# Kernel tuning notes

Measured on AMD Instinct MI355X. Metric: run time of the kernel, lower is better.

The kernel has to match this reference:

```python
import jax, jax.numpy as jnp
import numpy as np

B, N, F_IN, F_OUT = 8, 2048, 64, 64
ALPHA = 0.2  # LeakyReLU negative slope
LN_EPS = 1e-5
NEG_BIG = -9e15


def setup_inputs() -> dict:
    key = jax.random.key(0)
    ks = jax.random.split(key, 8)
    inp = {}
    inp["input"] = jax.random.normal(ks[0], (B, N, F_IN), dtype=jnp.float32)
    inp["adj"] = jax.random.randint(ks[1], (N, N), 0, 2, dtype=jnp.int32)
    # parameters (kaiming/xavier approximated with scaled normals)
    inp["W"] = jax.random.normal(ks[2], (F_IN, F_OUT), dtype=jnp.float32) * np.sqrt(2.0 / F_OUT)
    inp["a"] = jax.random.normal(ks[3], (2 * F_OUT, 1), dtype=jnp.float32) * np.sqrt(2.0 / (2 * F_OUT + 1))
    inp["node_weights"] = jax.random.normal(ks[4], (N,), dtype=jnp.float32)
    inp["node_bias"] = jnp.zeros((N,), dtype=jnp.float32)
    inp["ln_gamma"] = jnp.ones((F_OUT,), dtype=jnp.float32)
    inp["ln_beta"] = jnp.zeros((F_OUT,), dtype=jnp.float32)
    return inp


def reference(input, adj, W, a, node_weights, node_bias, ln_gamma, ln_beta):
    # eval mode: dropout is identity
    # node-wise affine + residual
    x = input * node_weights[None, :, None] + node_bias[None, :, None] + input
    # linear projection + LayerNorm over features
    h = jnp.matmul(x, W)  # [B, N, F_OUT]
    mu = jnp.mean(h, axis=-1, keepdims=True)
    var = jnp.mean(jnp.square(h - mu), axis=-1, keepdims=True)
    h = (h - mu) * jax.lax.rsqrt(var + LN_EPS) * ln_gamma + ln_beta
    # additive GAT scores WITHOUT materializing [B,N,N,2F]:
    # e_ij = LeakyReLU(h_i . a1 + h_j . a2), identical math to cat([h_i,h_j]) @ a
    a1 = a[:F_OUT, 0]
    a2 = a[F_OUT:, 0]
    s1 = jnp.einsum("bnf,f->bn", h, a1)  # [B, N]
    s2 = jnp.einsum("bnf,f->bn", h, a2)  # [B, N]
    e = jax.nn.leaky_relu(s1[:, :, None] + s2[:, None, :], negative_slope=ALPHA)
    # masked softmax over neighbors (last axis)
    mask = (adj > 0)[None, :, :]  # [1, N, N] broadcast over batch
    att = jax.nn.softmax(jnp.where(mask, e, NEG_BIG), axis=-1)
    # weighted aggregation + residual, then ELU (concat=True)
    h_prime = jnp.matmul(att, h) + h
    return jax.nn.elu(h_prime)
```

## Files before the change

### kernel.cpp

```cpp
#include <hip/hip_runtime.h>
#include <math.h>

#define Bb 8
#define Nn 2048
#define ALPHA 0.2f
#define LN_EPS 1e-5f
#define LOG2E 1.4426950408889634f

typedef __attribute__((ext_vector_type(8))) short short8;
typedef __attribute__((ext_vector_type(4))) float f32x4;
typedef __attribute__((ext_vector_type(4))) int int4v;

__device__ inline unsigned short f2bf(float f) {
    unsigned u = __builtin_bit_cast(unsigned, f);
    u += 0x7fffu + ((u >> 16) & 1u);
    return (unsigned short)(u >> 16);
}

__device__ __forceinline__ void gll16(const void* g, void* l) {
    __builtin_amdgcn_global_load_lds(
        (const __attribute__((address_space(1))) unsigned int*)g,
        (__attribute__((address_space(3))) unsigned int*)l, 16, 0, 0);
}

__global__ __launch_bounds__(256) void pack_mask(const int* __restrict__ adj,
                                                 unsigned int* __restrict__ bitsT) {
    int g = blockIdx.x * blockDim.x + threadIdx.x;
    int lane = threadIdx.x & 63;
    int pred = adj[g] > 0;
    unsigned long long b = __ballot(pred);
    if ((lane & 31) == 0) {
        unsigned w32 = (unsigned)(b >> (lane & 32));
        int i = g >> 11, w = (g >> 5) & 63;
        bitsT[((size_t)(i >> 4) * 64 + w) * 16 + (i & 15)] = w32;
    }
}

__global__ __launch_bounds__(64) void node_transform_mfma(
    const float* __restrict__ in, const float* __restrict__ W,
    const float* __restrict__ a, const float* __restrict__ nw,
    const float* __restrict__ nb, const float* __restrict__ gam,
    const float* __restrict__ bet,
    float* __restrict__ h, float* __restrict__ s1L, float* __restrict__ s2L,
    unsigned short* __restrict__ hT2)
{
    int lane = threadIdx.x;
    int am = lane & 15, ag = lane >> 4;
    int node0 = blockIdx.x * 16;
    int b = node0 >> 11;
    int n0 = node0 & (Nn - 1);

    short8 wf[4][2];
#pragma unroll
    for (int cb = 0; cb < 4; ++cb)
#pragma unroll
        for (int kh = 0; kh < 2; ++kh)
#pragma unroll
            for (int e = 0; e < 8; ++e)
                wf[cb][kh][e] = (short)f2bf(W[(kh * 32 + 8 * ag + e) * 64 + cb * 16 + am]);

    int nrow = n0 + am;
    float nwv = nw[nrow] + 1.0f, nbv = nb[nrow];
    const float* xrow = in + (size_t)(node0 + am) * 64 + 8 * ag;
    short8 xa0, xa1;
#pragma unroll
    for (int e = 0; e < 8; ++e) {
        xa0[e] = (short)f2bf(xrow[e] * nwv + nbv);
        xa1[e] = (short)f2bf(xrow[32 + e] * nwv + nbv);
    }

    f32x4 acc0 = {0,0,0,0}, acc1 = {0,0,0,0}, acc2 = {0,0,0,0}, acc3 = {0,0,0,0};
    acc0 = __builtin_amdgcn_mfma_f32_16x16x32_bf16(xa0, wf[0][0], acc0, 0, 0, 0);
    acc1 = __builtin_amdgcn_mfma_f32_16x16x32_bf16(xa0, wf[1][0], acc1, 0, 0, 0);
    acc2 = __builtin_amdgcn_mfma_f32_16x16x32_bf16(xa0, wf[2][0], acc2, 0, 0, 0);
    acc3 = __builtin_amdgcn_mfma_f32_16x16x32_bf16(xa0, wf[3][0], acc3, 0, 0, 0);
    acc0 = __builtin_amdgcn_mfma_f32_16x16x32_bf16(xa1, wf[0][1], acc0, 0, 0, 0);
    acc1 = __builtin_amdgcn_mfma_f32_16x16x32_bf16(xa1, wf[1][1], acc1, 0, 0, 0);
    acc2 = __builtin_amdgcn_mfma_f32_16x16x32_bf16(xa1, wf[2][1], acc2, 0, 0, 0);
    acc3 = __builtin_amdgcn_mfma_f32_16x16x32_bf16(xa1, wf[3][1], acc3, 0, 0, 0);

    float mu[4], rsq[4];
#pragma unroll
    for (int q = 0; q < 4; ++q) {
        float s = (acc0[q] + acc1[q]) + (acc2[q] + acc3[q]);
        s += __shfl_xor(s, 1, 64); s += __shfl_xor(s, 2, 64);
        s += __shfl_xor(s, 4, 64); s += __shfl_xor(s, 8, 64);
        mu[q] = s * (1.f / 64.f);
    }
#pragma unroll
    for (int q = 0; q < 4; ++q) {
        float d0 = acc0[q] - mu[q], d1 = acc1[q] - mu[q];
        float d2 = acc2[q] - mu[q], d3 = acc3[q] - mu[q];
        float ss = (d0 * d0 + d1 * d1) + (d2 * d2 + d3 * d3);
        ss += __shfl_xor(ss, 1, 64); ss += __shfl_xor(ss, 2, 64);
        ss += __shfl_xor(ss, 4, 64); ss += __shfl_xor(ss, 8, 64);
        rsq[q] = rsqrtf(ss * (1.f / 64.f) + LN_EPS);
    }
    float gl0 = gam[am], gl1 = gam[16 + am], gl2 = gam[32 + am], gl3 = gam[48 + am];
    float bl0 = bet[am], bl1 = bet[16 + am], bl2 = bet[32 + am], bl3 = bet[48 + am];
    f32x4 hn0, hn1, hn2, hn3;
#pragma unroll
    for (int q = 0; q < 4; ++q) {
        hn0[q] = (acc0[q] - mu[q]) * rsq[q] * gl0 + bl0;
        hn1[q] = (acc1[q] - mu[q]) * rsq[q] * gl1 + bl1;
        hn2[q] = (acc2[q] - mu[q]) * rsq[q] * gl2 + bl2;
        hn3[q] = (acc3[q] - mu[q]) * rsq[q] * gl3 + bl3;
    }

    float a10 = a[am], a11 = a[16 + am], a12 = a[32 + am], a13 = a[48 + am];
    float a20 = a[64 + am], a21 = a[80 + am], a22 = a[96 + am], a23 = a[112 + am];
    float s1p[4], s2p[4];
#pragma unroll
    for (int q = 0; q < 4; ++q) {
        float s1v = (hn0[q] * a10 + hn1[q] * a11) + (hn2[q] * a12 + hn3[q] * a13);
        float s2v = (hn0[q] * a20 + hn1[q] * a21) + (hn2[q] * a22 + hn3[q] * a23);
        s1v += __shfl_xor(s1v, 1, 64); s1v += __shfl_xor(s1v, 2, 64);
        s1v += __shfl_xor(s1v, 4, 64); s1v += __shfl_xor(s1v, 8, 64);
        s2v += __shfl_xor(s2v, 1, 64); s2v += __shfl_xor(s2v, 2, 64);
        s2v += __shfl_xor(s2v, 4, 64); s2v += __shfl_xor(s2v, 8, 64);
        s1p[q] = s1v; s2p[q] = s2v;
    }
    if (am == 0) {
#pragma unroll
        for (int q = 0; q < 4; ++q) {
            s1L[node0 + ag * 4 + q] = s1p[q] * LOG2E;
            s2L[node0 + ag * 4 + q] = s2p[q] * LOG2E;
        }
    }

#pragma unroll
    for (int q = 0; q < 4; ++q) {
        float* hp = h + (size_t)(node0 + ag * 4 + q) * 64 + am;
        hp[0] = hn0[q]; hp[16] = hn1[q]; hp[32] = hn2[q]; hp[48] = hn3[q];
    }

    int jw = n0 >> 5;
    int AG2 = ((n0 & 31) >> 3) + (ag >> 1);
    int e0 = (ag & 1) * 4;
    size_t fbase = ((size_t)((b * 64 + jw) * 4)) * 512 + (AG2 * 16 + am) * 8 + e0;
#pragma unroll
    for (int cb = 0; cb < 4; ++cb) {
        f32x4 hc = cb == 0 ? hn0 : cb == 1 ? hn1 : cb == 2 ? hn2 : hn3;
        unsigned short v[4] = {f2bf(hc[0]), f2bf(hc[1]), f2bf(hc[2]), f2bf(hc[3])};
        *(uint2*)&hT2[fbase + (size_t)cb * 512] = *(uint2*)v;
    }
}

__global__ __launch_bounds__(256, 4) void attention8(
    const unsigned short* __restrict__ hT2,
    const float* __restrict__ s1L, const float* __restrict__ s2L,
    const unsigned int* __restrict__ bitsT,
    float* __restrict__ pacc, float* __restrict__ pz)
{
    __shared__ __align__(16) unsigned short frag[2][4][4][512];
    __shared__ __align__(16) unsigned int mask_lds[2][32][16];
    __shared__ __align__(16) float s2l[1024];

    int t = threadIdx.x, wv = t >> 6, lane = t & 63;
    int am = lane & 15, ag = lane >> 4;
    int rr = wv & 1, js = wv >> 1;
    int bx = blockIdx.x, jh = blockIdx.y, b = blockIdx.z;

    float s1r = s1L[b * Nn + bx * 32 + rr * 16 + am];
    const unsigned short* slab = hT2 + (size_t)b * 131072;

    {
        const unsigned int* msrc = bitsT
            + ((size_t)(bx * 2 + (wv >> 1)) * 64 + jh * 32) * 16 + (wv & 1) * 256;
        gll16(msrc + lane * 4, &((unsigned int*)mask_lds)[wv * 256]);
        gll16(s2L + b * Nn + jh * 1024 + wv * 256 + lane * 4, &s2l[wv * 256]);
    }
    {
        const unsigned short* wsrc = slab + ((size_t)(jh * 32 + wv) * 4) * 512;
#pragma unroll
        for (int fb = 0; fb < 4; ++fb)
            gll16(wsrc + fb * 512 + lane * 8, &frag[0][wv][fb][0]);
    }
    asm volatile("s_waitcnt vmcnt(0)" ::: "memory");
    __builtin_amdgcn_s_barrier();

    f32x4 acc0 = {0,0,0,0}, acc1 = {0,0,0,0}, acc2 = {0,0,0,0}, acc3 = {0,0,0,0};
    f32x4 accz = {0,0,0,0};
    const short8 vone = {(short)0x3F80, (short)0x3F80, (short)0x3F80, (short)0x3F80,
                         (short)0x3F80, (short)0x3F80, (short)0x3F80, (short)0x3F80};

#pragma unroll
    for (int st = 0; st < 8; ++st) {
        if (st < 7) {
            const unsigned short* wsrc =
                slab + ((size_t)(jh * 32 + (st + 1) * 4 + wv) * 4) * 512;
#pragma unroll
            for (int fb = 0; fb < 4; ++fb)
                gll16(wsrc + fb * 512 + lane * 8, &frag[(st + 1) & 1][wv][fb][0]);
        }
#pragma unroll
        for (int wi = 0; wi < 2; ++wi) {
            int wls = js * 2 + wi;
            int wl = st * 4 + wls;
            unsigned wd = mask_lds[rr][wl][am];
            float4 sa = *(const float4*)&s2l[wl * 32 + 8 * ag];
            float4 sb = *(const float4*)&s2l[wl * 32 + 8 * ag + 4];
            float se[8] = {sa.x, sa.y, sa.z, sa.w, sb.x, sb.y, sb.z, sb.w};
            float p[8];
#pragma unroll
            for (int e = 0; e < 8; ++e) {
                float x = s1r + se[e];
                float lr = fmaxf(x, ALPHA * x);
                float ev = __builtin_amdgcn_exp2f(lr);
                p[e] = ((wd >> (8 * ag + e)) & 1u) ? ev : 0.f;
            }
            int4v aw;
            aw.x = __builtin_amdgcn_perm(__builtin_bit_cast(unsigned, p[1]),
                                         __builtin_bit_cast(unsigned, p[0]), 0x07060302u);
            aw.y = __builtin_amdgcn_perm(__builtin_bit_cast(unsigned, p[3]),
                                         __builtin_bit_cast(unsigned, p[2]), 0x07060302u);
            aw.z = __builtin_amdgcn_perm(__builtin_bit_cast(unsigned, p[5]),
                                         __builtin_bit_cast(unsigned, p[4]), 0x07060302u);
            aw.w = __builtin_amdgcn_perm(__builtin_bit_cast(unsigned, p[7]),
                                         __builtin_bit_cast(unsigned, p[6]), 0x07060302u);
            short8 af = __builtin_bit_cast(short8, aw);
            short8 f0 = *(const short8*)&frag[st & 1][wls][0][lane * 8];
            short8 f1 = *(const short8*)&frag[st & 1][wls][1][lane * 8];
            short8 f2 = *(const short8*)&frag[st & 1][wls][2][lane * 8];
            short8 f3 = *(const short8*)&frag[st & 1][wls][3][lane * 8];
            acc0 = __builtin_amdgcn_mfma_f32_16x16x32_bf16(af, f0, acc0, 0, 0, 0);
            acc1 = __builtin_amdgcn_mfma_f32_16x16x32_bf16(af, f1, acc1, 0, 0, 0);
            acc2 = __builtin_amdgcn_mfma_f32_16x16x32_bf16(af, f2, acc2, 0, 0, 0);
            acc3 = __builtin_amdgcn_mfma_f32_16x16x32_bf16(af, f3, acc3, 0, 0, 0);
            accz = __builtin_amdgcn_mfma_f32_16x16x32_bf16(af, vone, accz, 0, 0, 0);
        }
        asm volatile("s_waitcnt vmcnt(0)" ::: "memory");
        __builtin_amdgcn_s_barrier();
    }

    float* ep  = (float*)&frag[0][0][0][0];
    float* zep = (float*)&frag[1][0][0][0];
#pragma unroll
    for (int q = 0; q < 4; ++q) {
        int rloc = rr * 16 + 4 * ag + q;
        ep[(js * 32 + rloc) * 64 +  0 + am] = acc0[q];
        ep[(js * 32 + rloc) * 64 + 16 + am] = acc1[q];
        ep[(js * 32 + rloc) * 64 + 32 + am] = acc2[q];
        ep[(js * 32 + rloc) * 64 + 48 + am] = acc3[q];
        if (am == 0) zep[js * 32 + rloc] = accz[q];
    }
    __syncthreads();

    int rl = t >> 3, fo = (t & 7) * 8;
    float zsum = zep[rl] + zep[32 + rl];
    const float* e0p = &ep[rl * 64 + fo];
    const float* e1p = &ep[(32 + rl) * 64 + fo];
    size_t prow = (size_t)(b * 2 + jh) * 2048 + bx * 32 + rl;
    float4 v0, v1;
    v0.x = e0p[0] + e1p[0]; v0.y = e0p[1] + e1p[1];
    v0.z = e0p[2] + e1p[2]; v0.w = e0p[3] + e1p[3];
    v1.x = e0p[4] + e1p[4]; v1.y = e0p[5] + e1p[5];
    v1.z = e0p[6] + e1p[6]; v1.w = e0p[7] + e1p[7];
    *(float4*)&pacc[prow * 64 + fo]     = v0;
    *(float4*)&pacc[prow * 64 + fo + 4] = v1;
    if ((t & 7) == 0) pz[prow] = zsum;
}

__global__ __launch_bounds__(256) void combine(
    const float* __restrict__ pacc, const float* __restrict__ pz,
    const float* __restrict__ h, float* __restrict__ out)
{
    int u = blockIdx.x * 256 + threadIdx.x;
    int fq = u & 15, grow = u >> 4;
    int b = grow >> 11, i = grow & 2047;
    size_t p0 = ((size_t)(b * 2) * 2048 + i) * 64 + fq * 4;
    float4 a0 = *(const float4*)&pacc[p0];
    float4 a1 = *(const float4*)&pacc[p0 + (size_t)2048 * 64];
    float z = pz[(size_t)(b * 2) * 2048 + i] + pz[(size_t)(b * 2 + 1) * 2048 + i];
    float zinv = 1.f / z;
    size_t ob = (size_t)grow * 64 + fq * 4;
    float4 hv = *(const float4*)&h[ob];
    float4 o;
    o.x = (a0.x + a1.x) * zinv + hv.x; o.x = o.x > 0.f ? o.x : expm1f(o.x);
    o.y = (a0.y + a1.y) * zinv + hv.y; o.y = o.y > 0.f ? o.y : expm1f(o.y);
    o.z = (a0.z + a1.z) * zinv + hv.z; o.z = o.z > 0.f ? o.z : expm1f(o.z);
    o.w = (a0.w + a1.w) * zinv + hv.w; o.w = o.w > 0.f ? o.w : expm1f(o.w);
    *(float4*)&out[ob] = o;
}

extern "C" void kernel_launch(void* const* d_in, const int* in_sizes, int n_in,
                              void* d_out, int out_size, void* d_ws, size_t ws_size,
                              hipStream_t stream) {
    const float* in  = (const float*)d_in[0];
    const int*   adj = (const int*)d_in[1];
    const float* W   = (const float*)d_in[2];
    const float* a   = (const float*)d_in[3];
    const float* nw  = (const float*)d_in[4];
    const float* nb  = (const float*)d_in[5];
    const float* gam = (const float*)d_in[6];
    const float* bet = (const float*)d_in[7];
    float* out = (float*)d_out;

    char* ws = (char*)d_ws;
    float* h   = (float*)ws;
    float* s1L = (float*)(ws + (size_t)Bb * Nn * 64 * 4);
    float* s2L = s1L + (size_t)Bb * Nn;
    unsigned int* bitsT = (unsigned int*)(s2L + (size_t)Bb * Nn);
    unsigned short* hT2 = (unsigned short*)(bitsT + (size_t)Nn * Nn / 32);
    float* pacc = (float*)(hT2 + (size_t)Bb * 64 * Nn);
    float* pz   = pacc + (size_t)16 * 2048 * 64;

    hipLaunchKernelGGL(pack_mask, dim3(Nn * Nn / 256), dim3(256), 0, stream, adj, bitsT);
    hipLaunchKernelGGL(node_transform_mfma, dim3(Bb * Nn / 16), dim3(64), 0, stream,
                       in, W, a, nw, nb, gam, bet, h, s1L, s2L, hT2);
    hipLaunchKernelGGL(attention8, dim3(Nn / 32, 2, Bb), dim3(256), 0, stream,
                       hT2, s1L, s2L, bitsT, pacc, pz);
    hipLaunchKernelGGL(combine, dim3((Bb * Nn * 16) / 256), dim3(256), 0, stream,
                       pacc, pz, h, out);
}
```

Baseline: 36.07 us.

## Fuse mask packing with node transform and fold combine into attention

Mask packing and the node transform now run as one launch, with extra blocks handling adjacency rows through vectorized int4 loads and an LDS byte gather. The attention kernel drops the split over the neighbor dimension, so each block loops over all 2048 neighbors in 16 stages. It also applies the normalization, residual and ELU directly, which removes the partial-sum buffers and the separate combine kernel. In exchange there are half as many attention blocks (512 instead of 1024) with larger LDS use and the occupancy hint removed, which may reduce latency hiding.

```diff
diff --git a/kernel.cpp b/kernel.cpp
--- a/kernel.cpp
+++ b/kernel.cpp
@@ -23,30 +23,40 @@
         (__attribute__((address_space(3))) unsigned int*)l, 16, 0, 0);
 }
 
-__global__ __launch_bounds__(256) void pack_mask(const int* __restrict__ adj,
-                                                 unsigned int* __restrict__ bitsT) {
-    int g = blockIdx.x * blockDim.x + threadIdx.x;
-    int lane = threadIdx.x & 63;
-    int pred = adj[g] > 0;
-    unsigned long long b = __ballot(pred);
-    if ((lane & 31) == 0) {
-        unsigned w32 = (unsigned)(b >> (lane & 32));
-        int i = g >> 11, w = (g >> 5) & 63;
-        bitsT[((size_t)(i >> 4) * 64 + w) * 16 + (i & 15)] = w32;
-    }
-}
-
-__global__ __launch_bounds__(64) void node_transform_mfma(
+__global__ __launch_bounds__(256) void prep(
+    const int* __restrict__ adj,
     const float* __restrict__ in, const float* __restrict__ W,
     const float* __restrict__ a, const float* __restrict__ nw,
     const float* __restrict__ nb, const float* __restrict__ gam,
     const float* __restrict__ bet,
+    unsigned int* __restrict__ bitsT,
     float* __restrict__ h, float* __restrict__ s1L, float* __restrict__ s2L,
     unsigned short* __restrict__ hT2)
 {
-    int lane = threadIdx.x;
+    __shared__ unsigned char rowb[256];
+    int bid = blockIdx.x, t = threadIdx.x;
+
+    if (bid < Nn) {
+        int i = bid;
+        const int4* arow = (const int4*)(adj + (size_t)i * Nn);
+        int4 v0 = arow[t * 2], v1 = arow[t * 2 + 1];
+        unsigned by = (unsigned)(v0.x > 0)       | ((unsigned)(v0.y > 0) << 1)
+                    | ((unsigned)(v0.z > 0) << 2) | ((unsigned)(v0.w > 0) << 3)
+                    | ((unsigned)(v1.x > 0) << 4) | ((unsigned)(v1.y > 0) << 5)
+                    | ((unsigned)(v1.z > 0) << 6) | ((unsigned)(v1.w > 0) << 7);
+        rowb[t] = (unsigned char)by;
+        __syncthreads();
+        if (t < 64) {
+            unsigned w32;
+            __builtin_memcpy(&w32, &rowb[t * 4], 4);
+            bitsT[((size_t)(i >> 4) * 64 + t) * 16 + (i & 15)] = w32;
+        }
+        return;
+    }
+
+    int lane = t & 63, wv = t >> 6;
     int am = lane & 15, ag = lane >> 4;
-    int node0 = blockIdx.x * 16;
+    int node0 = (bid - Nn) * 64 + wv * 16;
     int b = node0 >> 11;
     int n0 = node0 & (Nn - 1);
 
@@ -146,36 +156,34 @@
     }
 }
 
-__global__ __launch_bounds__(256, 4) void attention8(
-    const unsigned short* __restrict__ hT2,
+__global__ __launch_bounds__(256) void attention9(
+    const float* __restrict__ h, const unsigned short* __restrict__ hT2,
     const float* __restrict__ s1L, const float* __restrict__ s2L,
-    const unsigned int* __restrict__ bitsT,
-    float* __restrict__ pacc, float* __restrict__ pz)
+    const unsigned int* __restrict__ bitsT, float* __restrict__ out)
 {
     __shared__ __align__(16) unsigned short frag[2][4][4][512];
-    __shared__ __align__(16) unsigned int mask_lds[2][32][16];
-    __shared__ __align__(16) float s2l[1024];
+    __shared__ __align__(16) unsigned int mask_lds[2][64][16];
+    __shared__ __align__(16) float s2l[2048];
 
     int t = threadIdx.x, wv = t >> 6, lane = t & 63;
     int am = lane & 15, ag = lane >> 4;
     int rr = wv & 1, js = wv >> 1;
-    int bx = blockIdx.x, jh = blockIdx.y, b = blockIdx.z;
+    int bx = blockIdx.x, b = blockIdx.y;
 
     float s1r = s1L[b * Nn + bx * 32 + rr * 16 + am];
+    const unsigned int* msrc = bitsT + (size_t)(bx * 2) * 1024;
+    const float* ssrc = s2L + b * Nn;
     const unsigned short* slab = hT2 + (size_t)b * 131072;
 
-    {
-        const unsigned int* msrc = bitsT
-            + ((size_t)(bx * 2 + (wv >> 1)) * 64 + jh * 32) * 16 + (wv & 1) * 256;
-        gll16(msrc + lane * 4, &((unsigned int*)mask_lds)[wv * 256]);
-        gll16(s2L + b * Nn + jh * 1024 + wv * 256 + lane * 4, &s2l[wv * 256]);
-    }
-    {
-        const unsigned short* wsrc = slab + ((size_t)(jh * 32 + wv) * 4) * 512;
-#pragma unroll
-        for (int fb = 0; fb < 4; ++fb)
-            gll16(wsrc + fb * 512 + lane * 8, &frag[0][wv][fb][0]);
-    }
+#pragma unroll
+    for (int k = 0; k < 2; ++k) {
+        int sl = wv * 2 + k;
+        gll16(msrc + sl * 256 + lane * 4, &((unsigned int*)mask_lds)[sl * 256]);
+        gll16(ssrc + sl * 256 + lane * 4, &s2l[sl * 256]);
+    }
+#pragma unroll
+    for (int fb = 0; fb < 4; ++fb)
+        gll16(slab + (size_t)(wv * 4 + fb) * 512 + lane * 8, &frag[0][wv][fb][0]);
     asm volatile("s_waitcnt vmcnt(0)" ::: "memory");
     __builtin_amdgcn_s_barrier();
 
@@ -185,13 +193,13 @@
                          (short)0x3F80, (short)0x3F80, (short)0x3F80, (short)0x3F80};
 
 #pragma unroll
-    for (int st = 0; st < 8; ++st) {
-        if (st < 7) {
-            const unsigned short* wsrc =
-                slab + ((size_t)(jh * 32 + (st + 1) * 4 + wv) * 4) * 512;
+    for (int st = 0; st < 16; ++st) {
+        if (st < 15) {
+            int gw = (st + 1) * 4 + wv;
 #pragma unroll
             for (int fb = 0; fb < 4; ++fb)
-                gll16(wsrc + fb * 512 + lane * 8, &frag[(st + 1) & 1][wv][fb][0]);
+                gll16(slab + (size_t)(gw * 4 + fb) * 512 + lane * 8,
+                      &frag[(st + 1) & 1][wv][fb][0]);
         }
 #pragma unroll
         for (int wi = 0; wi < 2; ++wi) {
@@ -247,40 +255,23 @@
     __syncthreads();
 
     int rl = t >> 3, fo = (t & 7) * 8;
-    float zsum = zep[rl] + zep[32 + rl];
+    float zinv = 1.f / (zep[rl] + zep[32 + rl]);
+    size_t base = ((size_t)(b * Nn + bx * 32 + rl)) * 64 + fo;
     const float* e0p = &ep[rl * 64 + fo];
     const float* e1p = &ep[(32 + rl) * 64 + fo];
-    size_t prow = (size_t)(b * 2 + jh) * 2048 + bx * 32 + rl;
-    float4 v0, v1;
-    v0.x = e0p[0] + e1p[0]; v0.y = e0p[1] + e1p[1];
-    v0.z = e0p[2] + e1p[2]; v0.w = e0p[3] + e1p[3];
-    v1.x = e0p[4] + e1p[4]; v1.y = e0p[5] + e1p[5];
-    v1.z = e0p[6] + e1p[6]; v1.w = e0p[7] + e1p[7];
-    *(float4*)&pacc[prow * 64 + fo]     = v0;
-    *(float4*)&pacc[prow * 64 + fo + 4] = v1;
-    if ((t & 7) == 0) pz[prow] = zsum;
-}
-
-__global__ __launch_bounds__(256) void combine(
-    const float* __restrict__ pacc, const float* __restrict__ pz,
-    const float* __restrict__ h, float* __restrict__ out)
-{
-    int u = blockIdx.x * 256 + threadIdx.x;
-    int fq = u & 15, grow = u >> 4;
-    int b = grow >> 11, i = grow & 2047;
-    size_t p0 = ((size_t)(b * 2) * 2048 + i) * 64 + fq * 4;
-    float4 a0 = *(const float4*)&pacc[p0];
-    float4 a1 = *(const float4*)&pacc[p0 + (size_t)2048 * 64];
-    float z = pz[(size_t)(b * 2) * 2048 + i] + pz[(size_t)(b * 2 + 1) * 2048 + i];
-    float zinv = 1.f / z;
-    size_t ob = (size_t)grow * 64 + fq * 4;
-    float4 hv = *(const float4*)&h[ob];
-    float4 o;
-    o.x = (a0.x + a1.x) * zinv + hv.x; o.x = o.x > 0.f ? o.x : expm1f(o.x);
-    o.y = (a0.y + a1.y) * zinv + hv.y; o.y = o.y > 0.f ? o.y : expm1f(o.y);
-    o.z = (a0.z + a1.z) * zinv + hv.z; o.z = o.z > 0.f ? o.z : expm1f(o.z);
-    o.w = (a0.w + a1.w) * zinv + hv.w; o.w = o.w > 0.f ? o.w : expm1f(o.w);
-    *(float4*)&out[ob] = o;
+    float4 h0 = *(const float4*)&h[base];
+    float4 h1 = *(const float4*)&h[base + 4];
+    float4 o0, o1;
+    o0.x = (e0p[0] + e1p[0]) * zinv + h0.x; o0.x = o0.x > 0.f ? o0.x : expm1f(o0.x);
+    o0.y = (e0p[1] + e1p[1]) * zinv + h0.y; o0.y = o0.y > 0.f ? o0.y : expm1f(o0.y);
+    o0.z = (e0p[2] + e1p[2]) * zinv + h0.z; o0.z = o0.z > 0.f ? o0.z : expm1f(o0.z);
+    o0.w = (e0p[3] + e1p[3]) * zinv + h0.w; o0.w = o0.w > 0.f ? o0.w : expm1f(o0.w);
+    o1.x = (e0p[4] + e1p[4]) * zinv + h1.x; o1.x = o1.x > 0.f ? o1.x : expm1f(o1.x);
+    o1.y = (e0p[5] + e1p[5]) * zinv + h1.y; o1.y = o1.y > 0.f ? o1.y : expm1f(o1.y);
+    o1.z = (e0p[6] + e1p[6]) * zinv + h1.z; o1.z = o1.z > 0.f ? o1.z : expm1f(o1.z);
+    o1.w = (e0p[7] + e1p[7]) * zinv + h1.w; o1.w = o1.w > 0.f ? o1.w : expm1f(o1.w);
+    *(float4*)&out[base] = o0;
+    *(float4*)&out[base + 4] = o1;
 }
 
 extern "C" void kernel_launch(void* const* d_in, const int* in_sizes, int n_in,
@@ -302,14 +293,9 @@
     float* s2L = s1L + (size_t)Bb * Nn;
     unsigned int* bitsT = (unsigned int*)(s2L + (size_t)Bb * Nn);
     unsigned short* hT2 = (unsigned short*)(bitsT + (size_t)Nn * Nn / 32);
-    float* pacc = (float*)(hT2 + (size_t)Bb * 64 * Nn);
-    float* pz   = pacc + (size_t)16 * 2048 * 64;
-
-    hipLaunchKernelGGL(pack_mask, dim3(Nn * Nn / 256), dim3(256), 0, stream, adj, bitsT);
-    hipLaunchKernelGGL(node_transform_mfma, dim3(Bb * Nn / 16), dim3(64), 0, stream,
-                       in, W, a, nw, nb, gam, bet, h, s1L, s2L, hT2);
-    hipLaunchKernelGGL(attention8, dim3(Nn / 32, 2, Bb), dim3(256), 0, stream,
-                       hT2, s1L, s2L, bitsT, pacc, pz);
-    hipLaunchKernelGGL(combine, dim3((Bb * Nn * 16) / 256), dim3(256), 0, stream,
-                       pacc, pz, h, out);
-}
+
+    hipLaunchKernelGGL(prep, dim3(Nn + Bb * Nn / 64), dim3(256), 0, stream,
+                       adj, in, W, a, nw, nb, gam, bet, bitsT, h, s1L, s2L, hT2);
+    hipLaunchKernelGGL(attention9, dim3(Nn / 32, Bb), dim3(256), 0, stream,
+                       h, hT2, s1L, s2L, bitsT, out);
+}
```

Result: faster. 33.49 us (-7.2%).
